# Optimization experiments

Hardware: AMD Instinct MI355X
Metric: run time of the kernel (lower is better)

## Reference

```python
import jax, jax.numpy as jnp
import numpy as np

B, N_PTS, M_ROIS = 2, 8192, 2048
C_IN, O, H, NS = 128, 256, 4, 32
RADIUS = 1.6
BN_EPS = 1e-5
SCALE = 10.0  # point cloud extent


def setup_inputs() -> dict:
    key = jax.random.key(0)
    ks = jax.random.split(key, 20)
    f32 = jnp.float32
    Cg = C_IN + 3  # grouper concats relative xyz to features

    def kaiming(k, shape, fan_in):
        return jax.random.normal(k, shape, f32) * np.sqrt(2.0 / fan_in)

    inp = {
        "xyz": jax.random.uniform(ks[0], (B, N_PTS, 3), f32) * SCALE,
        "new_xyz": jax.random.uniform(ks[1], (B, M_ROIS, 3), f32) * SCALE,
        "features": jax.random.normal(ks[2], (B, C_IN, N_PTS), f32),
        # conv1d (kernel=1, no bias) weights, torch layout (out, in)
        "pos_w": kaiming(ks[3], (O, 3), 3),
        "key_w": kaiming(ks[4], (O, Cg), Cg),
        "val_w1": kaiming(ks[5], (O, Cg), Cg),
        "bn1_g": jnp.ones((O,), f32), "bn1_b": jnp.zeros((O,), f32),
        "val_w2": kaiming(ks[6], (O, O), O),
        "bn2_g": jnp.ones((O,), f32), "bn2_b": jnp.zeros((O,), f32),
        "attn_w": kaiming(ks[7], (H, O), O),
        # sigmoid-gated coefficient linears (no bias)
        "kc_w": kaiming(ks[8], (O, O), O),
        "qc_w": kaiming(ks[9], (O, O), O),
        "qkc_w": kaiming(ks[10], (O, O), O),
        "vc_w": kaiming(ks[11], (O, O), O),
        # cls/reg weight MLPs: Linear(O,O//2)+ReLU, Linear(O//2,1)+Sigmoid
        "cls_w1": kaiming(ks[12], (O // 2, O), O), "cls_b1": jnp.zeros((O // 2,), f32),
        "cls_w2": kaiming(ks[13], (1, O // 2), O // 2), "cls_b2": jnp.zeros((1,), f32),
        "reg_w1": kaiming(ks[14], (O // 2, O), O), "reg_b1": jnp.zeros((O // 2,), f32),
        "reg_w2": kaiming(ks[15], (1, O // 2), O // 2), "reg_b2": jnp.zeros((1,), f32),
    }
    return inp


def _bn(x, g, b):
    # eval-mode BatchNorm1d with running_mean=0, running_var=1 (init state)
    return g[None, :, None] * (x * (1.0 / np.sqrt(1.0 + BN_EPS))) + b[None, :, None]


def _conv1x1(w, x):  # (O,C) x (M,C,NS) -> (M,O,NS)
    return jnp.einsum('oc,mcn->mon', w, x)


def _ball_group(pts, q):
    # ball query: first NS points within RADIUS of each query (pad with first hit)
    n_tot = pts.shape[0]
    d2 = jnp.sum((q[:, None, :] - pts[None, :, :]) ** 2, axis=-1)  # (M, Ntot)
    order = jnp.where(d2 < RADIUS ** 2, jnp.arange(n_tot, dtype=jnp.int32), n_tot)
    neg_vals, idx = jax.lax.top_k(-order, NS)  # smallest indices among in-ball pts
    valid = (-neg_vals) < n_tot
    idx = jnp.where(valid, idx, idx[:, :1])  # pad with first neighbor
    has_any = valid[:, :1]
    idx = jnp.where(has_any, idx, 0)  # empty balls -> point 0
    return idx, ~has_any[:, 0]


def reference(xyz, new_xyz, features, pos_w, key_w, val_w1, bn1_g, bn1_b,
              val_w2, bn2_g, bn2_b, attn_w, kc_w, qc_w, qkc_w, vc_w,
              cls_w1, cls_b1, cls_w2, cls_b2, reg_w1, reg_b1, reg_w2, reg_b2):
    pts = xyz.reshape(-1, 3)                                   # (Ntot, 3)
    feats = features.transpose(0, 2, 1).reshape(-1, C_IN)      # (Ntot, C)
    q = new_xyz.reshape(-1, 3)                                 # (M, 3)

    idx, empty_mask = _ball_group(pts, q)                      # (M, NS)
    gx = pts[idx] - q[:, None, :]                              # relative xyz (M,NS,3)
    gxt = gx.transpose(0, 2, 1)                                # (M,3,NS)
    gf = jnp.concatenate([gx, feats[idx]], axis=-1).transpose(0, 2, 1)  # (M,C+3,NS)

    pos = jax.nn.relu(_conv1x1(pos_w, gxt))                    # (M,O,NS)
    key = jax.nn.relu(_conv1x1(key_w, gf))                     # (M,O,NS)
    v = jax.nn.relu(_bn(_conv1x1(val_w1, gf), bn1_g, bn1_b))
    val = jax.nn.relu(_bn(_conv1x1(val_w2, v), bn2_g, bn2_b))  # (M,O,NS)
    pos_key = pos * key

    sig = jax.nn.sigmoid
    v_c = sig(pos.mean(2) @ vc_w.T)                            # (M,O)
    q_c = sig(pos.mean(2) @ qc_w.T)
    k_c = sig(key.mean(2) @ kc_w.T)
    qk_c = sig(pos_key.mean(2) @ qkc_w.T)

    val = val + pos * v_c[:, :, None]
    attn_emb = pos * q_c[:, :, None] + key * k_c[:, :, None] + pos_key * qk_c[:, :, None]
    attn = jax.nn.softmax(jnp.einsum('ho,mon->mhn', attn_w, attn_emb), axis=-1)  # (M,H,NS)

    m = val.shape[0]
    vh = val.reshape(m, H, O // H, NS)
    new_features = jnp.einsum('mhdn,mhn->mhd', vh, attn).reshape(m, O)  # (M,O)

    def gate(x, w1, b1, w2, b2):
        return sig(jax.nn.relu(x @ w1.T + b1) @ w2.T + b2)

    cls_features = new_features * gate(new_features, cls_w1, cls_b1, cls_w2, cls_b2)
    reg_features = new_features * gate(new_features, reg_w1, reg_b1, reg_w2, reg_b2)
    return new_features, cls_features, reg_features
```

## Files before the change

kernel.cpp:

```cpp
#include <hip/hip_runtime.h>

#define DI __device__ __forceinline__

typedef __attribute__((ext_vector_type(8))) short bf16x8;
typedef __attribute__((ext_vector_type(4))) short s16x4;
typedef __attribute__((ext_vector_type(4))) float f32x4;

DI short f2bs(float x){ unsigned u = __float_as_uint(x);
  return (short)((u + 0x7FFF + ((u >> 16) & 1)) >> 16); }
DI float bs2f(short s){ return __uint_as_float(((unsigned)(unsigned short)s) << 16); }
DI f32x4 MFMA(bf16x8 a, bf16x8 b, f32x4 c){
  return __builtin_amdgcn_mfma_f32_16x16x32_bf16(a, b, c, 0, 0, 0);
}

constexpr int NP   = 8192;
constexpr int NTOT = 16384;
constexpr int M    = 4096;
constexpr int C    = 128;
constexpr int O    = 256;
constexpr int NS   = 32;
constexpr int H    = 4;
constexpr int KP   = 160;
constexpr int GFS  = 168;
constexpr int VS   = 264;
constexpr float BNS = 0.99999500003749969f;

DI void copy_rows(short* __restrict__ dst, const short* __restrict__ src, int t){
  int row = t >> 3, s = (t & 7) * 8;
  const short* sp = src + row*VS + s;
  short* dp = dst + (size_t)row*O + s;
  #pragma unroll
  for(int j = 0; j < 4; j++)
    *(bf16x8*)(dp + j*64) = *(const bf16x8*)(sp + j*64);
}

__global__ __launch_bounds__(256) void k_transpose(const float* __restrict__ feat,
                                                   short* __restrict__ fT){
  __shared__ float tile[128][65];
  int blk = blockIdx.x;
  int b  = blk >> 7;
  int n0 = (blk & 127) << 6;
  int t = threadIdx.x;
  int nn = t & 63, c4 = t >> 6;
  const float* src = feat + (size_t)b * C * NP;
  for(int i = 0; i < 32; i++){
    int c = c4 * 32 + i;
    tile[c][nn] = src[(size_t)c * NP + n0 + nn];
  }
  __syncthreads();
  int c2 = t & 127, nb = t >> 7;
  for(int j = 0; j < 32; j++){
    int n = nb + j * 2;
    fT[((size_t)(b * NP + n0 + n)) * C + c2] = f2bs(tile[c2][n]);
  }
}

__global__ __launch_bounds__(256) void k_pack(
    const float* __restrict__ kw, const float* __restrict__ v1w,
    const float* __restrict__ v2w,
    const float* __restrict__ vcw, const float* __restrict__ qcw,
    const float* __restrict__ kcw, const float* __restrict__ qkcw,
    const float* __restrict__ cw1, const float* __restrict__ rw1,
    short* __restrict__ keyP, short* __restrict__ v1P,
    short* __restrict__ v2b,
    short* __restrict__ gw,
    short* __restrict__ cw1b, short* __restrict__ rw1b)
{
  int i = blockIdx.x * 256 + threadIdx.x;
  if(i < O * KP){
    int o = i / KP, k = i % KP;
    float a = 0.0f, b = 0.0f;
    if(k < 128){ a = kw[o*131 + 3 + k]; b = v1w[o*131 + 3 + k]; }
    else if(k < 131){ a = kw[o*131 + (k - 128)]; b = v1w[o*131 + (k - 128)]; }
    keyP[i] = f2bs(a);
    v1P[i]  = f2bs(b);
  }
  if(i < O * O){
    v2b[i] = f2bs(v2w[i]);
    gw[0*O*O + i] = f2bs(vcw[i]);
    gw[1*O*O + i] = f2bs(qcw[i]);
    gw[2*O*O + i] = f2bs(kcw[i]);
    gw[3*O*O + i] = f2bs(qkcw[i]);
  }
  if(i < (O/2) * O){
    cw1b[i] = f2bs(cw1[i]);
    rw1b[i] = f2bs(rw1[i]);
  }
}

__global__ __launch_bounds__(64) void k_ballq(const float* __restrict__ xyz,
                                              const float* __restrict__ nxyz,
                                              int* __restrict__ idxo,
                                              float* __restrict__ gxo){
#pragma clang fp contract(off)
  int m = blockIdx.x;
  int lane = threadIdx.x;
  float qx = nxyz[m*3+0], qy = nxyz[m*3+1], qz = nxyz[m*3+2];
  __shared__ int sel[NS];
  int cnt = 0;
  for(int base = 0; base < NTOT; base += 64){
    int p = base + lane;
    float dx = qx - xyz[p*3+0], dy = qy - xyz[p*3+1], dz = qz - xyz[p*3+2];
    float d2 = dx*dx + dy*dy;
    d2 = d2 + dz*dz;
    bool pred = d2 < 2.56f;
    unsigned long long bal = __ballot(pred);
    if(pred){
      int pos = cnt + __popcll(bal & ((1ull << lane) - 1ull));
      if(pos < NS) sel[pos] = p;
    }
    cnt += __popcll(bal);
    if(cnt >= NS) break;
  }
  __syncthreads();
  if(lane < NS){
    int s = 0;
    if(cnt > 0) s = (lane < cnt) ? sel[lane] : sel[0];
    idxo[m*NS + lane] = s;
    gxo[(m*NS+lane)*3+0] = xyz[s*3+0] - qx;
    gxo[(m*NS+lane)*3+1] = xyz[s*3+1] - qy;
    gxo[(m*NS+lane)*3+2] = xyz[s*3+2] - qz;
  }
}

__global__ __launch_bounds__(256, 5) void k_conv(
    const short* __restrict__ fT,
    const short* __restrict__ keyP, const short* __restrict__ v1P,
    const short* __restrict__ v2b,
    const float* __restrict__ posw,
    const float* __restrict__ g1, const float* __restrict__ b1,
    const float* __restrict__ g2, const float* __restrict__ b2,
    const int* __restrict__ idxw, const float* __restrict__ gxw,
    short* __restrict__ keyo, short* __restrict__ valo,
    float* __restrict__ mPos, float* __restrict__ mKey, float* __restrict__ mPK,
    int q0)
{
  int lq = blockIdx.x, q = q0 + lq, t = threadIdx.x;
  int w = t >> 6, l = t & 63;
  int col = l & 15, kq = l >> 4;
  int ro = w * 64;
  __shared__ __align__(16) short gf[NS * GFS];
  __shared__ __align__(16) short vbuf[NS * VS];
  __shared__ float gxs[NS * 4];
  __shared__ int  sel[NS];
  if(t < NS){
    sel[t] = idxw[q*NS + t];
    gxs[t*4+0] = gxw[(q*NS+t)*3+0];
    gxs[t*4+1] = gxw[(q*NS+t)*3+1];
    gxs[t*4+2] = gxw[(q*NS+t)*3+2];
    gxs[t*4+3] = 0.0f;
  }
  __syncthreads();
  for(int i = 0; i < 8; i++){
    int n = w*8 + i;
    int p = sel[n];
    *(unsigned*)&gf[n*GFS + l*2] = *(const unsigned*)(fT + (size_t)p * C + l*2);
  }
  {
    int n = t & 31, kk = (t >> 5) * 4;
    for(int j = 0; j < 4; j++){
      int k = kk + j;
      float v = (k < 3) ? gxs[n*4 + k] : 0.0f;
      gf[n*GFS + 128 + k] = f2bs(v);
    }
  }
  __syncthreads();

  float posR[4][2][4];
  for(int mt=0;mt<4;mt++) for(int r=0;r<4;r++){
    int o = ro + mt*16 + kq*4 + r;
    float w0 = posw[o*3+0], w1 = posw[o*3+1], w2 = posw[o*3+2];
    for(int nt=0;nt<2;nt++){
      int n = nt*16 + col;
      posR[mt][nt][r] = fmaxf(w0*gxs[n*4+0] + w1*gxs[n*4+1] + w2*gxs[n*4+2], 0.0f);
    }
  }

  f32x4 acc[4][2];
  const f32x4 vzero = {0.0f, 0.0f, 0.0f, 0.0f};

  for(int mt=0;mt<4;mt++) for(int nt=0;nt<2;nt++) acc[mt][nt] = vzero;
  for(int ks = 0; ks < 5; ks++){
    bf16x8 b0 = *(const bf16x8*)&gf[col*GFS + ks*32 + kq*8];
    bf16x8 b1v = *(const bf16x8*)&gf[(16+col)*GFS + ks*32 + kq*8];
    for(int mt = 0; mt < 4; mt++){
      bf16x8 a = *(const bf16x8*)(keyP + (size_t)(ro + mt*16 + col)*KP + ks*32 + kq*8);
      acc[mt][0] = MFMA(a, b0, acc[mt][0]);
      acc[mt][1] = MFMA(a, b1v, acc[mt][1]);
    }
  }
  float mS[4][4][3];
  for(int mt=0;mt<4;mt++){
    for(int nt=0;nt<2;nt++){
      s16x4 pk;
      for(int r=0;r<4;r++){
        float v = fmaxf(acc[mt][nt][r], 0.0f);
        pk[r] = f2bs(v);
        if(nt == 0){ mS[mt][r][0] = posR[mt][0][r];  mS[mt][r][1] = v;
                     mS[mt][r][2] = posR[mt][0][r]*v; }
        else       { mS[mt][r][0] += posR[mt][1][r]; mS[mt][r][1] += v;
                     mS[mt][r][2] += posR[mt][1][r]*v; }
      }
      int n = nt*16 + col;
      *(s16x4*)&vbuf[n*VS + ro + mt*16 + kq*4] = pk;
    }
  }
  __syncthreads();
  copy_rows(keyo + (size_t)lq*NS*O, vbuf, t);
  for(int mt=0;mt<4;mt++) for(int r=0;r<4;r++){
    float sp = mS[mt][r][0], sk = mS[mt][r][1], spk = mS[mt][r][2];
    for(int msk=1; msk<16; msk<<=1){
      sp += __shfl_xor(sp, msk); sk += __shfl_xor(sk, msk); spk += __shfl_xor(spk, msk);
    }
    if(col == 0){
      int o = ro + mt*16 + kq*4 + r;
      mPos[lq*O+o] = sp  * 0.03125f;
      mKey[lq*O+o] = sk  * 0.03125f;
      mPK [lq*O+o] = spk * 0.03125f;
    }
  }

  for(int mt=0;mt<4;mt++) for(int nt=0;nt<2;nt++) acc[mt][nt] = vzero;
  for(int ks = 0; ks < 5; ks++){
    bf16x8 b0 = *(const bf16x8*)&gf[col*GFS + ks*32 + kq*8];
    bf16x8 b1v = *(const bf16x8*)&gf[(16+col)*GFS + ks*32 + kq*8];
    for(int mt = 0; mt < 4; mt++){
      bf16x8 a = *(const bf16x8*)(v1P + (size_t)(ro + mt*16 + col)*KP + ks*32 + kq*8);
      acc[mt][0] = MFMA(a, b0, acc[mt][0]);
      acc[mt][1] = MFMA(a, b1v, acc[mt][1]);
    }
  }
  __syncthreads();
  for(int mt=0;mt<4;mt++){
    int o0 = ro + mt*16 + kq*4;
    float gg[4], bb[4];
    for(int r=0;r<4;r++){ gg[r] = g1[o0+r]; bb[r] = b1[o0+r]; }
    for(int nt=0;nt<2;nt++){
      s16x4 pk;
      for(int r=0;r<4;r++)
        pk[r] = f2bs(fmaxf(gg[r]*(acc[mt][nt][r] * BNS) + bb[r], 0.0f));
      int n = nt*16 + col;
      *(s16x4*)&vbuf[n*VS + o0] = pk;
    }
  }
  __syncthreads();

  for(int mt=0;mt<4;mt++) for(int nt=0;nt<2;nt++) acc[mt][nt] = vzero;
  for(int ks = 0; ks < 8; ks++){
    bf16x8 b0 = *(const bf16x8*)&vbuf[col*VS + ks*32 + kq*8];
    bf16x8 b1v = *(const bf16x8*)&vbuf[(16+col)*VS + ks*32 + kq*8];
    for(int mt = 0; mt < 4; mt++){
      bf16x8 a = *(const bf16x8*)(v2b + (size_t)(ro + mt*16 + col)*O + ks*32 + kq*8);
      acc[mt][0] = MFMA(a, b0, acc[mt][0]);
      acc[mt][1] = MFMA(a, b1v, acc[mt][1]);
    }
  }
  s16x4 valS[4][2];
  for(int mt=0;mt<4;mt++){
    int o0 = ro + mt*16 + kq*4;
    float gg[4], bb[4];
    for(int r=0;r<4;r++){ gg[r] = g2[o0+r]; bb[r] = b2[o0+r]; }
    for(int nt=0;nt<2;nt++)
      for(int r=0;r<4;r++)
        valS[mt][nt][r] = f2bs(fmaxf(gg[r]*(acc[mt][nt][r] * BNS) + bb[r], 0.0f));
  }
  __syncthreads();
  for(int mt=0;mt<4;mt++) for(int nt=0;nt<2;nt++){
    int n = nt*16 + col;
    *(s16x4*)&vbuf[n*VS + ro + mt*16 + kq*4] = valS[mt][nt];
  }
  __syncthreads();
  copy_rows(valo + (size_t)lq*NS*O, vbuf, t);
}

__global__ __launch_bounds__(256) void k_gates(
    const float* __restrict__ mPos, const float* __restrict__ mKey,
    const float* __restrict__ mPK, const short* __restrict__ gw,
    float* __restrict__ gates)
{
  int t = threadIdx.x, w = t >> 6, l = t & 63, col = l & 15, kq = l >> 4;
  int lq0 = blockIdx.x * 16;
  const float* A  = (w < 2) ? mPos : ((w == 2) ? mKey : mPK);
  const short* Wg = gw + (size_t)w * O * O;
  f32x4 acc[16];
  const f32x4 vzero = {0.0f,0.0f,0.0f,0.0f};
  for(int i=0;i<16;i++) acc[i] = vzero;
  for(int ks = 0; ks < 8; ks++){
    union { bf16x8 v; short e[8]; } u;
    const float* ap = A + (size_t)(lq0 + col)*O + ks*32 + kq*8;
    for(int j = 0; j < 8; j++) u.e[j] = f2bs(ap[j]);
    for(int nt = 0; nt < 16; nt++){
      bf16x8 bv = *(const bf16x8*)(Wg + (size_t)(nt*16 + col)*O + ks*32 + kq*8);
      acc[nt] = MFMA(u.v, bv, acc[nt]);
    }
  }
  for(int nt=0;nt<16;nt++) for(int r=0;r<4;r++){
    int lqq = lq0 + kq*4 + r;
    int oo = nt*16 + col;
    gates[((size_t)lqq*4 + w)*O + oo] = 1.0f / (1.0f + expf(-acc[nt][r]));
  }
}

__global__ __launch_bounds__(256) void k_attn(
    const short* __restrict__ keyw, const short* __restrict__ valw,
    const float* __restrict__ gxw, const float* __restrict__ posw,
    const float* __restrict__ attw, const float* __restrict__ gates,
    float* __restrict__ outNF, int q0)
{
  int lq = blockIdx.x, q = q0 + lq, t = threadIdx.x;
  __shared__ float emL[O * 33];
  __shared__ float attnL[H * NS];
  __shared__ float gxs[NS * 3];
  __shared__ float partial[256];
  if(t < 96) gxs[t] = gxw[q*96 + t];
  float vc  = gates[((size_t)lq*4 + 0)*O + t];
  float qc  = gates[((size_t)lq*4 + 1)*O + t];
  float kc  = gates[((size_t)lq*4 + 2)*O + t];
  float qkc = gates[((size_t)lq*4 + 3)*O + t];
  float pw0 = posw[t*3+0], pw1 = posw[t*3+1], pw2 = posw[t*3+2];
  __syncthreads();
  float posr[NS];
  for(int n = 0; n < NS; n++)
    posr[n] = fmaxf(pw0*gxs[n*3] + pw1*gxs[n*3+1] + pw2*gxs[n*3+2], 0.0f);
  for(int n = 0; n < NS; n++){
    float k = bs2f(keyw[((size_t)lq*NS + n)*O + t]);
    emL[t*33 + n] = posr[n]*qc + k*kc + posr[n]*k*qkc;
  }
  __syncthreads();
  {
    int idx = t & 127, h = idx >> 5, n = idx & 31, half = t >> 7;
    float s = 0;
    const float* aw = attw + h*O + half*128;
    for(int o = 0; o < 128; o++) s += aw[o] * emL[(half*128 + o)*33 + n];
    partial[t] = s;
  }
  __syncthreads();
  if(t < 128){
    int h = t >> 5, n = t & 31;
    float s = partial[t] + partial[t + 128];
    float mx = s;
    for(int msk=1; msk<32; msk<<=1) mx = fmaxf(mx, __shfl_xor(mx, msk));
    float e = expf(s - mx);
    float sum = e;
    for(int msk=1; msk<32; msk<<=1) sum += __shfl_xor(sum, msk);
    attnL[h*NS + n] = e / sum;
  }
  __syncthreads();
  int h = t >> 6;
  float nf = 0;
  for(int n = 0; n < NS; n++){
    float v = bs2f(valw[((size_t)lq*NS + n)*O + t]);
    nf += (v + posr[n]*vc) * attnL[h*NS + n];
  }
  outNF[(size_t)q*O + t] = nf;
}

__global__ __launch_bounds__(256) void k_fgate(
    const float* __restrict__ nf,
    const short* __restrict__ cw1b, const float* __restrict__ cb1,
    const float* __restrict__ cw2, const float* __restrict__ cb2,
    const short* __restrict__ rw1b, const float* __restrict__ rb1,
    const float* __restrict__ rw2, const float* __restrict__ rb2,
    float* __restrict__ outC, float* __restrict__ outR)
{
  int t = threadIdx.x, w = t >> 6, l = t & 63, col = l & 15, kq = l >> 4;
  int q0 = blockIdx.x * 64;
  __shared__ float sC[64], sR[64];
  f32x4 acc[16];
  const f32x4 vzero = {0.0f,0.0f,0.0f,0.0f};
  for(int i=0;i<16;i++) acc[i] = vzero;
  int arow = q0 + w*16 + col;
  for(int ks = 0; ks < 8; ks++){
    union { bf16x8 v; short e[8]; } u;
    const float* ap = nf + (size_t)arow*O + ks*32 + kq*8;
    for(int j = 0; j < 8; j++) u.e[j] = f2bs(ap[j]);
    for(int nt = 0; nt < 16; nt++){
      const short* W1 = (nt < 8) ? cw1b : rw1b;
      int j = (nt & 7)*16 + col;
      bf16x8 bv = *(const bf16x8*)(W1 + (size_t)j*O + ks*32 + kq*8);
      acc[nt] = MFMA(u.v, bv, acc[nt]);
    }
  }
  for(int r = 0; r < 4; r++){
    float pc = 0, pr = 0;
    for(int nt = 0; nt < 8; nt++){
      int j = nt*16 + col;
      pc += fmaxf(acc[nt][r] + cb1[j], 0.0f) * cw2[j];
    }
    for(int nt = 8; nt < 16; nt++){
      int j = (nt - 8)*16 + col;
      pr += fmaxf(acc[nt][r] + rb1[j], 0.0f) * rw2[j];
    }
    for(int msk=1; msk<16; msk<<=1){ pc += __shfl_xor(pc, msk); pr += __shfl_xor(pr, msk); }
    if(col == 0){
      int qq = w*16 + kq*4 + r;
      sC[qq] = 1.0f / (1.0f + expf(-(pc + cb2[0])));
      sR[qq] = 1.0f / (1.0f + expf(-(pr + rb2[0])));
    }
  }
  __syncthreads();
  for(int qq = 0; qq < 64; qq++){
    float nv = nf[(size_t)(q0 + qq)*O + t];
    outC[(size_t)(q0 + qq)*O + t] = nv * sC[qq];
    outR[(size_t)(q0 + qq)*O + t] = nv * sR[qq];
  }
}

extern "C" void kernel_launch(void* const* d_in, const int* in_sizes, int n_in,
                              void* d_out, int out_size, void* d_ws, size_t ws_size,
                              hipStream_t stream)
{
  const float* xyz  = (const float*)d_in[0];
  const float* nxyz = (const float*)d_in[1];
  const float* feat = (const float*)d_in[2];
  const float* posw = (const float*)d_in[3];
  const float* keyw = (const float*)d_in[4];
  const float* v1w  = (const float*)d_in[5];
  const float* bn1g = (const float*)d_in[6];
  const float* bn1b = (const float*)d_in[7];
  const float* v2w  = (const float*)d_in[8];
  const float* bn2g = (const float*)d_in[9];
  const float* bn2b = (const float*)d_in[10];
  const float* attw = (const float*)d_in[11];
  const float* kcw  = (const float*)d_in[12];
  const float* qcw  = (const float*)d_in[13];
  const float* qkcw = (const float*)d_in[14];
  const float* vcw  = (const float*)d_in[15];
  const float* cw1  = (const float*)d_in[16];
  const float* cb1  = (const float*)d_in[17];
  const float* cw2  = (const float*)d_in[18];
  const float* cb2  = (const float*)d_in[19];
  const float* rw1  = (const float*)d_in[20];
  const float* rb1  = (const float*)d_in[21];
  const float* rw2  = (const float*)d_in[22];
  const float* rb2  = (const float*)d_in[23];

  const size_t fixedB = 12000000;
  const size_t perQ   = 40960;
  int Q = 64;
  for(int cand : {4096, 2048, 1024, 512, 256, 128}){
    if(fixedB + (size_t)cand*perQ <= ws_size){ Q = cand; break; }
  }

  char* p = (char*)d_ws;
  auto alloc = [&](size_t bytes){ char* r = p; p += (bytes + 255) & ~size_t(255); return r; };
  short* fT    = (short*)alloc((size_t)NTOT*C*2);
  short* keyP  = (short*)alloc((size_t)O*KP*2);
  short* v1P   = (short*)alloc((size_t)O*KP*2);
  short* v2b   = (short*)alloc((size_t)O*O*2);
  short* gw    = (short*)alloc((size_t)4*O*O*2);
  short* cw1b  = (short*)alloc((size_t)(O/2)*O*2);
  short* rw1b  = (short*)alloc((size_t)(O/2)*O*2);
  int*   idxw  = (int*)  alloc((size_t)M*NS*4);
  float* gxw   = (float*)alloc((size_t)M*NS*3*4);
  short* keyo  = (short*)alloc((size_t)Q*NS*O*2);
  short* valo  = (short*)alloc((size_t)Q*NS*O*2);
  float* mPos  = (float*)alloc((size_t)Q*O*4);
  float* mKey  = (float*)alloc((size_t)Q*O*4);
  float* mPK   = (float*)alloc((size_t)Q*O*4);
  float* gates = (float*)alloc((size_t)Q*4*O*4);

  float* outNF = (float*)d_out;
  float* outC  = outNF + (size_t)M*O;
  float* outR  = outC  + (size_t)M*O;

  k_transpose<<<256, 256, 0, stream>>>(feat, fT);
  k_pack     <<<256, 256, 0, stream>>>(keyw, v1w, v2w, vcw, qcw, kcw, qkcw, cw1, rw1,
                                       keyP, v1P, v2b, gw, cw1b, rw1b);
  k_ballq    <<<M,   64,  0, stream>>>(xyz, nxyz, idxw, gxw);
  for(int q0 = 0; q0 < M; q0 += Q){
    k_conv  <<<Q,    256, 0, stream>>>(fT, keyP, v1P, v2b,
                                       posw, bn1g, bn1b, bn2g, bn2b,
                                       idxw, gxw, keyo, valo, mPos, mKey, mPK, q0);
    k_gates <<<Q/16, 256, 0, stream>>>(mPos, mKey, mPK, gw, gates);
    k_attn  <<<Q,    256, 0, stream>>>(keyo, valo, gxw, posw, attw, gates, outNF, q0);
  }
  k_fgate   <<<M/64, 256, 0, stream>>>(outNF, cw1b, cb1, cw2, cb2, rw1b, rb1, rw2, rb2, outC, outR);
}
```

Baseline: 408.7 us.

## Process two queries per conv block to reuse weight fragments across 64 columns

Each k_conv block now handles two ROI queries (64 grouped points) instead of one. Every weight A-fragment loaded from global memory then feeds four MFMA column tiles instead of two, halving weight traffic per query. The key and value outputs are written straight from registers as packed 8-byte stores rather than staged through shared memory and copied out, which removes several barriers. The kernel also reorders the value1 and key convolutions, computes the pos term inline, and lowers the launch-bounds occupancy hint from 5 to 2. The cost is a larger accumulator array, more shared memory per block and fewer resident blocks, plus less coalesced global stores.

```diff
diff --git a/kernel.cpp b/kernel.cpp
--- a/kernel.cpp
+++ b/kernel.cpp
@@ -5,10 +5,14 @@
 typedef __attribute__((ext_vector_type(8))) short bf16x8;
 typedef __attribute__((ext_vector_type(4))) short s16x4;
 typedef __attribute__((ext_vector_type(4))) float f32x4;
+typedef __attribute__((ext_vector_type(2))) unsigned int u32x2;
 
 DI short f2bs(float x){ unsigned u = __float_as_uint(x);
   return (short)((u + 0x7FFF + ((u >> 16) & 1)) >> 16); }
 DI float bs2f(short s){ return __uint_as_float(((unsigned)(unsigned short)s) << 16); }
+DI unsigned pack2(float a, float b){
+  return (unsigned)(unsigned short)f2bs(a) | ((unsigned)(unsigned short)f2bs(b) << 16);
+}
 DI f32x4 MFMA(bf16x8 a, bf16x8 b, f32x4 c){
   return __builtin_amdgcn_mfma_f32_16x16x32_bf16(a, b, c, 0, 0, 0);
 }
@@ -24,15 +28,6 @@
 constexpr int GFS  = 168;
 constexpr int VS   = 264;
 constexpr float BNS = 0.99999500003749969f;
-
-DI void copy_rows(short* __restrict__ dst, const short* __restrict__ src, int t){
-  int row = t >> 3, s = (t & 7) * 8;
-  const short* sp = src + row*VS + s;
-  short* dp = dst + (size_t)row*O + s;
-  #pragma unroll
-  for(int j = 0; j < 4; j++)
-    *(bf16x8*)(dp + j*64) = *(const bf16x8*)(sp + j*64);
-}
 
 __global__ __launch_bounds__(256) void k_transpose(const float* __restrict__ feat,
                                                    short* __restrict__ fT){
@@ -123,7 +118,7 @@
   }
 }
 
-__global__ __launch_bounds__(256, 5) void k_conv(
+__global__ __launch_bounds__(256, 2) void k_conv(
     const short* __restrict__ fT,
     const short* __restrict__ keyP, const short* __restrict__ v1P,
     const short* __restrict__ v2b,
@@ -135,142 +130,138 @@
     float* __restrict__ mPos, float* __restrict__ mKey, float* __restrict__ mPK,
     int q0)
 {
-  int lq = blockIdx.x, q = q0 + lq, t = threadIdx.x;
+  int lq2 = blockIdx.x, t = threadIdx.x;
   int w = t >> 6, l = t & 63;
   int col = l & 15, kq = l >> 4;
   int ro = w * 64;
-  __shared__ __align__(16) short gf[NS * GFS];
-  __shared__ __align__(16) short vbuf[NS * VS];
-  __shared__ float gxs[NS * 4];
-  __shared__ int  sel[NS];
-  if(t < NS){
-    sel[t] = idxw[q*NS + t];
-    gxs[t*4+0] = gxw[(q*NS+t)*3+0];
-    gxs[t*4+1] = gxw[(q*NS+t)*3+1];
-    gxs[t*4+2] = gxw[(q*NS+t)*3+2];
+  __shared__ __align__(16) short gf[64 * GFS];
+  __shared__ __align__(16) short vst[64 * VS];
+  __shared__ float gxs[64 * 4];
+  __shared__ int  sel[64];
+  int qg0 = q0 + lq2 * 2;
+  if(t < 64){
+    int qi = t >> 5, n = t & 31;
+    int gq = qg0 + qi;
+    sel[t] = idxw[gq*NS + n];
+    gxs[t*4+0] = gxw[(gq*NS+n)*3+0];
+    gxs[t*4+1] = gxw[(gq*NS+n)*3+1];
+    gxs[t*4+2] = gxw[(gq*NS+n)*3+2];
     gxs[t*4+3] = 0.0f;
   }
   __syncthreads();
-  for(int i = 0; i < 8; i++){
-    int n = w*8 + i;
+  for(int i = 0; i < 16; i++){
+    int n = w*16 + i;
     int p = sel[n];
     *(unsigned*)&gf[n*GFS + l*2] = *(const unsigned*)(fT + (size_t)p * C + l*2);
   }
   {
-    int n = t & 31, kk = (t >> 5) * 4;
-    for(int j = 0; j < 4; j++){
-      int k = kk + j;
+    int n = t & 63, j0 = (t >> 6) * 8;
+    for(int j = 0; j < 8; j++){
+      int k = j0 + j;
       float v = (k < 3) ? gxs[n*4 + k] : 0.0f;
       gf[n*GFS + 128 + k] = f2bs(v);
     }
   }
   __syncthreads();
 
-  float posR[4][2][4];
-  for(int mt=0;mt<4;mt++) for(int r=0;r<4;r++){
-    int o = ro + mt*16 + kq*4 + r;
-    float w0 = posw[o*3+0], w1 = posw[o*3+1], w2 = posw[o*3+2];
-    for(int nt=0;nt<2;nt++){
-      int n = nt*16 + col;
-      posR[mt][nt][r] = fmaxf(w0*gxs[n*4+0] + w1*gxs[n*4+1] + w2*gxs[n*4+2], 0.0f);
-    }
-  }
-
-  f32x4 acc[4][2];
+  f32x4 acc[4][4];
   const f32x4 vzero = {0.0f, 0.0f, 0.0f, 0.0f};
 
-  for(int mt=0;mt<4;mt++) for(int nt=0;nt<2;nt++) acc[mt][nt] = vzero;
+  for(int mt=0;mt<4;mt++) for(int nt=0;nt<4;nt++) acc[mt][nt] = vzero;
   for(int ks = 0; ks < 5; ks++){
-    bf16x8 b0 = *(const bf16x8*)&gf[col*GFS + ks*32 + kq*8];
-    bf16x8 b1v = *(const bf16x8*)&gf[(16+col)*GFS + ks*32 + kq*8];
-    for(int mt = 0; mt < 4; mt++){
-      bf16x8 a = *(const bf16x8*)(keyP + (size_t)(ro + mt*16 + col)*KP + ks*32 + kq*8);
-      acc[mt][0] = MFMA(a, b0, acc[mt][0]);
-      acc[mt][1] = MFMA(a, b1v, acc[mt][1]);
-    }
-  }
-  float mS[4][4][3];
-  for(int mt=0;mt<4;mt++){
-    for(int nt=0;nt<2;nt++){
-      s16x4 pk;
-      for(int r=0;r<4;r++){
-        float v = fmaxf(acc[mt][nt][r], 0.0f);
-        pk[r] = f2bs(v);
-        if(nt == 0){ mS[mt][r][0] = posR[mt][0][r];  mS[mt][r][1] = v;
-                     mS[mt][r][2] = posR[mt][0][r]*v; }
-        else       { mS[mt][r][0] += posR[mt][1][r]; mS[mt][r][1] += v;
-                     mS[mt][r][2] += posR[mt][1][r]*v; }
-      }
-      int n = nt*16 + col;
-      *(s16x4*)&vbuf[n*VS + ro + mt*16 + kq*4] = pk;
-    }
-  }
-  __syncthreads();
-  copy_rows(keyo + (size_t)lq*NS*O, vbuf, t);
-  for(int mt=0;mt<4;mt++) for(int r=0;r<4;r++){
-    float sp = mS[mt][r][0], sk = mS[mt][r][1], spk = mS[mt][r][2];
-    for(int msk=1; msk<16; msk<<=1){
-      sp += __shfl_xor(sp, msk); sk += __shfl_xor(sk, msk); spk += __shfl_xor(spk, msk);
-    }
-    if(col == 0){
-      int o = ro + mt*16 + kq*4 + r;
-      mPos[lq*O+o] = sp  * 0.03125f;
-      mKey[lq*O+o] = sk  * 0.03125f;
-      mPK [lq*O+o] = spk * 0.03125f;
-    }
-  }
-
-  for(int mt=0;mt<4;mt++) for(int nt=0;nt<2;nt++) acc[mt][nt] = vzero;
-  for(int ks = 0; ks < 5; ks++){
-    bf16x8 b0 = *(const bf16x8*)&gf[col*GFS + ks*32 + kq*8];
-    bf16x8 b1v = *(const bf16x8*)&gf[(16+col)*GFS + ks*32 + kq*8];
+    bf16x8 bf[4];
+    for(int nt=0;nt<4;nt++)
+      bf[nt] = *(const bf16x8*)&gf[(nt*16+col)*GFS + ks*32 + kq*8];
     for(int mt = 0; mt < 4; mt++){
       bf16x8 a = *(const bf16x8*)(v1P + (size_t)(ro + mt*16 + col)*KP + ks*32 + kq*8);
-      acc[mt][0] = MFMA(a, b0, acc[mt][0]);
-      acc[mt][1] = MFMA(a, b1v, acc[mt][1]);
-    }
-  }
-  __syncthreads();
+      for(int nt=0;nt<4;nt++) acc[mt][nt] = MFMA(a, bf[nt], acc[mt][nt]);
+    }
+  }
   for(int mt=0;mt<4;mt++){
     int o0 = ro + mt*16 + kq*4;
     float gg[4], bb[4];
     for(int r=0;r<4;r++){ gg[r] = g1[o0+r]; bb[r] = b1[o0+r]; }
-    for(int nt=0;nt<2;nt++){
+    for(int nt=0;nt<4;nt++){
       s16x4 pk;
       for(int r=0;r<4;r++)
         pk[r] = f2bs(fmaxf(gg[r]*(acc[mt][nt][r] * BNS) + bb[r], 0.0f));
-      int n = nt*16 + col;
-      *(s16x4*)&vbuf[n*VS + o0] = pk;
-    }
-  }
-  __syncthreads();
-
-  for(int mt=0;mt<4;mt++) for(int nt=0;nt<2;nt++) acc[mt][nt] = vzero;
+      *(s16x4*)&vst[(nt*16+col)*VS + o0] = pk;
+    }
+  }
+
+  for(int mt=0;mt<4;mt++) for(int nt=0;nt<4;nt++) acc[mt][nt] = vzero;
+  for(int ks = 0; ks < 5; ks++){
+    bf16x8 bf[4];
+    for(int nt=0;nt<4;nt++)
+      bf[nt] = *(const bf16x8*)&gf[(nt*16+col)*GFS + ks*32 + kq*8];
+    for(int mt = 0; mt < 4; mt++){
+      bf16x8 a = *(const bf16x8*)(keyP + (size_t)(ro + mt*16 + col)*KP + ks*32 + kq*8);
+      for(int nt=0;nt<4;nt++) acc[mt][nt] = MFMA(a, bf[nt], acc[mt][nt]);
+    }
+  }
+  for(int mt=0;mt<4;mt++){
+    int o0 = ro + mt*16 + kq*4;
+    float pw[4][3];
+    for(int r=0;r<4;r++){ pw[r][0]=posw[(o0+r)*3+0]; pw[r][1]=posw[(o0+r)*3+1];
+                          pw[r][2]=posw[(o0+r)*3+2]; }
+    for(int qi=0; qi<2; qi++){
+      float sp[4]={0,0,0,0}, sk[4]={0,0,0,0}, spk[4]={0,0,0,0};
+      for(int h=0; h<2; h++){
+        int nt = qi*2 + h;
+        int n  = nt*16 + col;
+        float gx0 = gxs[n*4+0], gx1 = gxs[n*4+1], gx2 = gxs[n*4+2];
+        float kvv[4];
+        for(int r=0;r<4;r++){
+          float kk = fmaxf(acc[mt][nt][r], 0.0f);
+          kvv[r] = kk;
+          float pv = fmaxf(pw[r][0]*gx0 + pw[r][1]*gx1 + pw[r][2]*gx2, 0.0f);
+          sp[r] += pv; sk[r] += kk; spk[r] += pv*kk;
+        }
+        int lql = lq2*2 + qi;
+        int nn = h*16 + col;
+        u32x2 pk2 = { pack2(kvv[0], kvv[1]), pack2(kvv[2], kvv[3]) };
+        *(u32x2*)&keyo[((size_t)lql*NS + nn)*O + o0] = pk2;
+      }
+      for(int r=0;r<4;r++){
+        float a = sp[r], b = sk[r], c = spk[r];
+        for(int msk=1; msk<16; msk<<=1){
+          a += __shfl_xor(a, msk); b += __shfl_xor(b, msk); c += __shfl_xor(c, msk);
+        }
+        if(col == 0){
+          int lql = lq2*2 + qi;
+          mPos[(size_t)lql*O + o0 + r] = a * 0.03125f;
+          mKey[(size_t)lql*O + o0 + r] = b * 0.03125f;
+          mPK [(size_t)lql*O + o0 + r] = c * 0.03125f;
+        }
+      }
+    }
+  }
+  __syncthreads();
+
+  for(int mt=0;mt<4;mt++) for(int nt=0;nt<4;nt++) acc[mt][nt] = vzero;
   for(int ks = 0; ks < 8; ks++){
-    bf16x8 b0 = *(const bf16x8*)&vbuf[col*VS + ks*32 + kq*8];
-    bf16x8 b1v = *(const bf16x8*)&vbuf[(16+col)*VS + ks*32 + kq*8];
+    bf16x8 bf[4];
+    for(int nt=0;nt<4;nt++)
+      bf[nt] = *(const bf16x8*)&vst[(nt*16+col)*VS + ks*32 + kq*8];
     for(int mt = 0; mt < 4; mt++){
       bf16x8 a = *(const bf16x8*)(v2b + (size_t)(ro + mt*16 + col)*O + ks*32 + kq*8);
-      acc[mt][0] = MFMA(a, b0, acc[mt][0]);
-      acc[mt][1] = MFMA(a, b1v, acc[mt][1]);
-    }
-  }
-  s16x4 valS[4][2];
+      for(int nt=0;nt<4;nt++) acc[mt][nt] = MFMA(a, bf[nt], acc[mt][nt]);
+    }
+  }
   for(int mt=0;mt<4;mt++){
     int o0 = ro + mt*16 + kq*4;
     float gg[4], bb[4];
     for(int r=0;r<4;r++){ gg[r] = g2[o0+r]; bb[r] = b2[o0+r]; }
-    for(int nt=0;nt<2;nt++)
+    for(int nt=0;nt<4;nt++){
+      float vv[4];
       for(int r=0;r<4;r++)
-        valS[mt][nt][r] = f2bs(fmaxf(gg[r]*(acc[mt][nt][r] * BNS) + bb[r], 0.0f));
-  }
-  __syncthreads();
-  for(int mt=0;mt<4;mt++) for(int nt=0;nt<2;nt++){
-    int n = nt*16 + col;
-    *(s16x4*)&vbuf[n*VS + ro + mt*16 + kq*4] = valS[mt][nt];
-  }
-  __syncthreads();
-  copy_rows(valo + (size_t)lq*NS*O, vbuf, t);
+        vv[r] = fmaxf(gg[r]*(acc[mt][nt][r] * BNS) + bb[r], 0.0f);
+      int lql = lq2*2 + (nt>>1);
+      int nn  = (nt&1)*16 + col;
+      u32x2 pk2 = { pack2(vv[0], vv[1]), pack2(vv[2], vv[3]) };
+      *(u32x2*)&valo[((size_t)lql*NS + nn)*O + o0] = pk2;
+    }
+  }
 }
 
 __global__ __launch_bounds__(256) void k_gates(
@@ -469,7 +460,7 @@
                                        keyP, v1P, v2b, gw, cw1b, rw1b);
   k_ballq    <<<M,   64,  0, stream>>>(xyz, nxyz, idxw, gxw);
   for(int q0 = 0; q0 < M; q0 += Q){
-    k_conv  <<<Q,    256, 0, stream>>>(fT, keyP, v1P, v2b,
+    k_conv  <<<Q/2,  256, 0, stream>>>(fT, keyP, v1P, v2b,
                                        posw, bn1g, bn1b, bn2g, bn2b,
                                        idxw, gxw, keyo, valo, mPos, mKey, mPK, q0);
     k_gates <<<Q/16, 256, 0, stream>>>(mPos, mKey, mPK, gw, gates);
```

Result: no change. 409.1 us (+0.1%).
